# Performance work log

Hardware: AMD Instinct MI355X
Metric: run time of the kernel (lower is better)

## Reference

```python
import jax, jax.numpy as jnp
import numpy as np

FOUR_PI = 4.0 * np.pi
BIG = 1e10


def winding_numbers(points, tris):
    """Generalized winding number of `points` [B,N,3] w.r.t. triangle soup
    `tris` [B,F,3,3], via the Van Oosterom-Strackee solid-angle formula."""
    # vectors from each query point to the three triangle corners: [B,N,F,3]
    a = tris[:, None, :, 0, :] - points[:, :, None, :]
    b = tris[:, None, :, 1, :] - points[:, :, None, :]
    c = tris[:, None, :, 2, :] - points[:, :, None, :]
    la = jnp.linalg.norm(a, axis=-1)
    lb = jnp.linalg.norm(b, axis=-1)
    lc = jnp.linalg.norm(c, axis=-1)
    det = jnp.sum(a * jnp.cross(b, c), axis=-1)  # scalar triple product [B,N,F]
    denom = (la * lb * lc
             + jnp.sum(a * b, axis=-1) * lc
             + jnp.sum(b * c, axis=-1) * la
             + jnp.sum(c * a, axis=-1) * lb)
    omega = 2.0 * jnp.arctan2(det, denom)  # solid angle per triangle
    return jnp.sum(omega, axis=-1) / FOUR_PI  # [B,N]


def pairwise_dist(x, y):
    """Euclidean distances between clouds x [B,N1,3] and y [B,N2,3] -> [B,N1,N2]."""
    sq = (jnp.sum(x * x, -1)[:, :, None]
          + jnp.sum(y * y, -1)[:, None, :]
          - 2.0 * jnp.einsum('bnd,bmd->bnm', x, y))
    return jnp.sqrt(jnp.maximum(sq, 0.0))


def setup_inputs() -> dict:
    key = jax.random.key(0)
    k1, k2, k3 = jax.random.split(key, 3)
    B, N, F = 2, 6890, 3
    NF = 2000
    v1 = jax.random.normal(k1, (B, N, 3), dtype=jnp.float32)
    v2 = jax.random.normal(k2, (B, N, 3), dtype=jnp.float32) + 0.5
    faces = jax.random.randint(k3, (NF, 3), 0, N, dtype=jnp.int32)
    return {"v1": v1, "v2": v2, "faces": faces}


def _masked_stats(row_min, mask):
    # row_min [B,K] minimum distances; mask [B,K] interior flags
    any_in = jnp.any(mask, axis=1)                                   # [B]
    mx = jnp.max(jnp.where(mask, row_min, -BIG), axis=1)
    cnt = jnp.sum(mask, axis=1).astype(row_min.dtype)
    mn = jnp.sum(jnp.where(mask, row_min, 0.0), axis=1) / jnp.maximum(cnt, 1.0)
    zero = jnp.zeros_like(mx)
    return jnp.where(any_in, mx, zero), jnp.where(any_in, mn, zero)


def reference(v1, v2, faces):
    # triangle soups (no mouth-closing: 'smpl' path): [B,F,3,3]
    t1 = v1[:, faces, :]
    t2 = v2[:, faces, :]
    interior_v1 = winding_numbers(v1, t2) >= 0.99  # [B,N1]
    interior_v2 = winding_numbers(v2, t1) >= 0.99  # [B,N2]
    d = pairwise_dist(v1, v2)                      # [B,N1,N2]
    min_dist = jnp.min(d, axis=(1, 2))             # [B]
    row_min = jnp.min(d, axis=2)                   # [B,N1] dist of each v1 to v2
    col_min = jnp.min(d, axis=1)                   # [B,N2] dist of each v2 to v1
    max_12, mean_12 = _masked_stats(row_min, interior_v1)
    max_21, mean_21 = _masked_stats(col_min, interior_v2)
    # stacked [5,B]: min_dist, max_v1_in_v2, mean_v1_in_v2, max_v2_in_v1, mean_v2_in_v1
    return jnp.stack([min_dist, max_12, mean_12, max_21, mean_21], axis=0)
```

## Files before the change

kernel.cpp:

```cpp
#include <hip/hip_runtime.h>
#include <math.h>

#define B_     2
#define N_     6890
#define NF_    2000
#define NFP_   2048
#define NPT_   6912
#define OPP7_  7168
#define TCG_   16
#define OCG_   7
#define NTILE_ (4 * (TCG_ + OCG_) * 27)
#define GRID_  2048

typedef float v2f __attribute__((ext_vector_type(2)));
#define VFMA(a,b,c) __builtin_elementwise_fma((v2f)(a), (v2f)(b), (v2f)(c))

__device__ __forceinline__ float atan2_o2pi(float y, float x) {
    float ax = __builtin_fabsf(x);
    float ay = __builtin_fabsf(y);
    float mx = fmaxf(ax, ay);
    float mn = fminf(ax, ay);
    bool  big = mn > 0.41421356f * mx;
    float num = big ? (mn - mx) : mn;
    float den = big ? (mn + mx) : mx;
    float t   = num * __builtin_amdgcn_rcpf(den);
    float z   = t * t;
    float p   = fmaf(fmaf(fmaf(1.2817932e-2f, z, -2.2087019e-2f), z,
                          3.1795514e-2f), z, -5.3051037e-2f);
    float r   = fmaf(t, fmaf(z, p, 0.15915494309f), big ? 0.125f : 0.0f);
    r = (ay > ax)  ? 0.25f - r : r;
    r = (x < 0.0f) ? 0.5f  - r : r;
    return copysignf(r, y);
}

__global__ void prep_kernel(const float* __restrict__ v1, const float* __restrict__ v2,
                            const int* __restrict__ faces,
                            float4* __restrict__ pw1, float4* __restrict__ pw2,
                            float4* __restrict__ st1, float4* __restrict__ st2,
                            float* __restrict__ tbl1, float* __restrict__ tbl2) {
    int tid = blockIdx.x * 256 + threadIdx.x;

    if (tid < B_ * NPT_) {
        int b = tid / NPT_, n = tid - b * NPT_;
        float4 q1 = make_float4(0.f, 0.f, 0.f, 0.f), q2 = q1;
        if (n < N_) {
            float x1 = v1[(b*N_+n)*3+0], y1 = v1[(b*N_+n)*3+1], z1 = v1[(b*N_+n)*3+2];
            float x2 = v2[(b*N_+n)*3+0], y2 = v2[(b*N_+n)*3+1], z2 = v2[(b*N_+n)*3+2];
            q1 = make_float4(x1, y1, z1, fmaf(x1,x1, fmaf(y1,y1, z1*z1)));
            q2 = make_float4(x2, y2, z2, fmaf(x2,x2, fmaf(y2,y2, z2*z2)));
        }
        pw1[tid] = q1; pw2[tid] = q2;
    }

    if (tid < B_ * OPP7_) {
        int b = tid / OPP7_, n = tid - b * OPP7_;
        float4 q1 = make_float4(0.f, 0.f, 0.f, 1e30f), q2 = q1;
        if (n < N_) {
            float x1 = v1[(b*N_+n)*3+0], y1 = v1[(b*N_+n)*3+1], z1 = v1[(b*N_+n)*3+2];
            float x2 = v2[(b*N_+n)*3+0], y2 = v2[(b*N_+n)*3+1], z2 = v2[(b*N_+n)*3+2];
            q1 = make_float4(-2.f*x1, -2.f*y1, -2.f*z1, fmaf(x1,x1, fmaf(y1,y1, z1*z1)));
            q2 = make_float4(-2.f*x2, -2.f*y2, -2.f*z2, fmaf(x2,x2, fmaf(y2,y2, z2*z2)));
        }
        st1[tid] = q1; st2[tid] = q2;
    }

    if (tid < 2 * B_ * NFP_) {
        int src = tid >> 12;
        int rr  = tid & (B_ * NFP_ - 1);
        int b   = rr >> 11;
        int f   = rr & (NFP_ - 1);
        const float* V = src ? v2 : v1;
        float Ax=1.f,Ay=1.f,Az=1.f,Bx=1.f,By=1.f,Bz=1.f,Cx=1.f,Cy=1.f,Cz=1.f;
        if (f < NF_) {
            int i0 = faces[f*3+0], i1 = faces[f*3+1], i2 = faces[f*3+2];
            Ax=V[(b*N_+i0)*3+0]; Ay=V[(b*N_+i0)*3+1]; Az=V[(b*N_+i0)*3+2];
            Bx=V[(b*N_+i1)*3+0]; By=V[(b*N_+i1)*3+1]; Bz=V[(b*N_+i1)*3+2];
            Cx=V[(b*N_+i2)*3+0]; Cy=V[(b*N_+i2)*3+1]; Cz=V[(b*N_+i2)*3+2];
        }
        float Sx = (Ay*Bz - Az*By) + (By*Cz - Bz*Cy) + (Cy*Az - Cz*Ay);
        float Sy = (Az*Bx - Ax*Bz) + (Bz*Cx - Bx*Cz) + (Cz*Ax - Cx*Az);
        float Sz = (Ax*By - Ay*Bx) + (Bx*Cy - By*Cx) + (Cx*Ay - Cy*Ax);
        float det0 = Ax*(By*Cz - Bz*Cy) + Ay*(Bz*Cx - Bx*Cz) + Az*(Bx*Cy - By*Cx);
        float na = Ax*Ax+Ay*Ay+Az*Az, nb = Bx*Bx+By*By+Bz*Bz, nc = Cx*Cx+Cy*Cy+Cz*Cz;
        float qab = Ax*Bx+Ay*By+Az*Bz, qbc = Bx*Cx+By*Cy+Bz*Cz, qca = Cx*Ax+Cy*Ay+Cz*Az;
        float* o = (src ? tbl2 : tbl1) + ((b << 11) + f) * 20;
        o[0]=Ax;  o[1]=Ay;  o[2]=Az;  o[3]=Bx;  o[4]=By;  o[5]=Bz;
        o[6]=Cx;  o[7]=Cy;  o[8]=Cz;  o[9]=-Sx; o[10]=-Sy; o[11]=-Sz;
        o[12]=det0; o[13]=na; o[14]=nb; o[15]=nc;
        o[16]=qab;  o[17]=qbc; o[18]=qca; o[19]=0.f;
    }
}

__global__ __launch_bounds__(256) void mega_kernel(
        const float4* __restrict__ pw1, const float4* __restrict__ pw2,
        const float* __restrict__ tbl1, const float* __restrict__ tbl2,
        const float4* __restrict__ st1, const float4* __restrict__ st2,
        float* __restrict__ part, float* __restrict__ rmp) {
    __shared__ float4 ptsd[512];
    int t = threadIdx.x, wid = t >> 6, lane = t & 63;
    int pbase = (wid << 7) + lane;
    int srcl = (lane + 1) & 63;

    for (int tile = blockIdx.x; tile < NTILE_; tile += GRID_) {
        int g = tile / 23, o = tile - g * 23;
        __syncthreads();

        if (o < TCG_) {
            int wb   = g * TCG_ + o;
            int pgrp = wb % 27;
            int r    = wb / 27;
            int cg   = r & 15, db = r >> 4;
            int b = db & 1, dir = db >> 1;

            const float4* pw  = dir ? pw2 : pw1;
            const float*  tbl = dir ? tbl1 : tbl2;

            float4 P0 = pw[b * NPT_ + pgrp * 256 + t];
            ptsd[pbase]      = P0;
            ptsd[pbase + 64] = P0;

            const float4* rpA = (const float4*)(tbl + (size_t)(b*NFP_ + cg*128 +   0 + lane)*20);
            const float4* rpB = (const float4*)(tbl + (size_t)(b*NFP_ + cg*128 +  64 + lane)*20);
            float4 a0 = rpA[0], a1 = rpA[1], a2 = rpA[2], a3 = rpA[3], a4 = rpA[4];
            float4 b0 = rpB[0], b1 = rpB[1], b2 = rpB[2], b3 = rpB[3], b4 = rpB[4];
            v2f cAx = {a0.x,b0.x}, cAy = {a0.y,b0.y}, cAz = {a0.z,b0.z};
            v2f cBx = {a0.w,b0.w}, cBy = {a1.x,b1.x}, cBz = {a1.y,b1.y};
            v2f cCx = {a1.z,b1.z}, cCy = {a1.w,b1.w}, cCz = {a2.x,b2.x};
            v2f cSx = {a2.y,b2.y}, cSy = {a2.z,b2.z}, cSz = {a2.w,b2.w};
            v2f cD0 = {a3.x,b3.x}, cNa = {a3.y,b3.y}, cNb = {a3.z,b3.z}, cNc = {a3.w,b3.w};
            v2f cQab= {a4.x,b4.x}, cQbc= {a4.y,b4.y}, cQca= {a4.z,b4.z};
            __syncthreads();

            const float4* mypts = ptsd + pbase;
            float acc = 0.f;
            #pragma unroll 4
            for (int k = 0; k < 64; ++k) {
                float4 P = mypts[k];
                v2f px = P.x, py = P.y, pz = P.z, sv = P.w;
                v2f dAp = VFMA(cAx, px, VFMA(cAy, py, cAz * pz));
                v2f dBp = VFMA(cBx, px, VFMA(cBy, py, cBz * pz));
                v2f dCp = VFMA(cCx, px, VFMA(cCy, py, cCz * pz));
                v2f det = VFMA(cSx, px, VFMA(cSy, py, VFMA(cSz, pz, cD0)));
                v2f la2 = VFMA((v2f)(-2.f), dAp, cNa + sv);
                v2f lb2 = VFMA((v2f)(-2.f), dBp, cNb + sv);
                v2f lc2 = VFMA((v2f)(-2.f), dCp, cNc + sv);
                v2f la, lb, lc;
                la.x = __builtin_amdgcn_sqrtf(fmaxf(la2.x, 0.f));
                la.y = __builtin_amdgcn_sqrtf(fmaxf(la2.y, 0.f));
                lb.x = __builtin_amdgcn_sqrtf(fmaxf(lb2.x, 0.f));
                lb.y = __builtin_amdgcn_sqrtf(fmaxf(lb2.y, 0.f));
                lc.x = __builtin_amdgcn_sqrtf(fmaxf(lc2.x, 0.f));
                lc.y = __builtin_amdgcn_sqrtf(fmaxf(lc2.y, 0.f));
                v2f dab = (cQab + sv) - (dAp + dBp);
                v2f dbc = (cQbc + sv) - (dBp + dCp);
                v2f dca = (cQca + sv) - (dCp + dAp);
                v2f denom = VFMA(VFMA(la, lb, dab), lc, VFMA(dbc, la, dca * lb));
                float g0 = atan2_o2pi(det.x, denom.x);
                float g1 = atan2_o2pi(det.y, denom.y);
                acc += g0 + g1;
                acc = __shfl(acc, srcl, 64);
            }
            part[(db*TCG_ + cg)*NPT_ + pgrp*256 + t] = acc;
        } else {
            int rb   = g * OCG_ + (o - TCG_);
            int pgrp = rb % 27;
            int r    = rb / 27;
            int ocg  = r % OCG_, db = r / OCG_;
            int b = db & 1, dir = db >> 1;

            const float4* pw = dir ? pw2 : pw1;
            const float4* st = dir ? st1 : st2;

            float4 P0 = pw[b * NPT_ + pgrp * 256 + t];
            ptsd[pbase]      = P0;
            ptsd[pbase + 64] = P0;

            const float4* qb = st + b * OPP7_ + ocg * 1024;
#define LQ(j) float4 q##j = qb[j*64 + lane];
            LQ(0) LQ(1) LQ(2) LQ(3) LQ(4) LQ(5) LQ(6) LQ(7)
            LQ(8) LQ(9) LQ(10) LQ(11) LQ(12) LQ(13) LQ(14) LQ(15)
#undef LQ
            __syncthreads();

            const float4* mypts = ptsd + pbase;
            float m = 3.4e38f;
            #pragma unroll 2
            for (int k = 0; k < 64; ++k) {
                float4 P = mypts[k];
                float s = P.w;
#define DD(j) float d##j = fmaf(q##j.x,P.x, fmaf(q##j.y,P.y, fmaf(q##j.z,P.z, q##j.w)));
                DD(0) DD(1) DD(2) DD(3) DD(4) DD(5) DD(6) DD(7)
                DD(8) DD(9) DD(10) DD(11) DD(12) DD(13) DD(14) DD(15)
#undef DD
                float e0 = fminf(d0,d1),  e1 = fminf(d2,d3),  e2 = fminf(d4,d5),  e3 = fminf(d6,d7);
                float e4 = fminf(d8,d9),  e5 = fminf(d10,d11), e6 = fminf(d12,d13), e7 = fminf(d14,d15);
                float f0 = fminf(e0,e1), f1 = fminf(e2,e3), f2 = fminf(e4,e5), f3 = fminf(e6,e7);
                float h  = fminf(fminf(f0,f1), fminf(f2,f3));
                m = fminf(m, h + s);
                m = __shfl(m, srcl, 64);
            }
            rmp[(db*OCG_ + ocg)*NPT_ + pgrp*256 + t] = m;
        }
    }
}

__global__ __launch_bounds__(256) void fold_kernel(
        const float* __restrict__ part, const float* __restrict__ rmp,
        float4* __restrict__ pstat) {
    int pg = blockIdx.x % 27, db = blockIdx.x / 27;
    int t = threadIdx.x, n = pg * 256 + t;

    float ws = 0.f;
    #pragma unroll
    for (int g = 0; g < TCG_; ++g) ws += part[(db*TCG_ + g)*NPT_ + n];
    float rv = 3.4e38f;
    #pragma unroll
    for (int g = 0; g < OCG_; ++g) rv = fminf(rv, rmp[(db*OCG_ + g)*NPT_ + n]);

    bool valid = n < N_;
    float d = sqrtf(rv);
    bool msk = valid && (ws >= 0.99f);
    float v_min = valid ? d : 3.4e38f;
    float v_max = msk ? d : -3.4e38f;
    float v_sum = msk ? d : 0.f;
    float v_cnt = msk ? 1.f : 0.f;

    #pragma unroll
    for (int off = 32; off; off >>= 1) {
        v_min = fminf(v_min, __shfl_down(v_min, off, 64));
        v_max = fmaxf(v_max, __shfl_down(v_max, off, 64));
        v_sum += __shfl_down(v_sum, off, 64);
        v_cnt += __shfl_down(v_cnt, off, 64);
    }
    __shared__ float4 sred[4];
    int wid = t >> 6, lane = t & 63;
    if (lane == 0) sred[wid] = make_float4(v_min, v_max, v_sum, v_cnt);
    __syncthreads();
    if (t == 0) {
        float4 a = sred[0], bb = sred[1], c = sred[2], dd = sred[3];
        pstat[db*27 + pg] = make_float4(
            fminf(fminf(a.x, bb.x), fminf(c.x, dd.x)),
            fmaxf(fmaxf(a.y, bb.y), fmaxf(c.y, dd.y)),
            (a.z + bb.z) + (c.z + dd.z),
            (a.w + bb.w) + (c.w + dd.w));
    }
}

__global__ void final_kernel(const float4* __restrict__ pstat, float* __restrict__ out) {
    int t = threadIdx.x, wid = t >> 6, lane = t & 63;
    float4 v = make_float4(3.4e38f, -3.4e38f, 0.f, 0.f);
    if (lane < 27) v = pstat[wid*27 + lane];
    #pragma unroll
    for (int off = 32; off; off >>= 1) {
        v.x = fminf(v.x, __shfl_down(v.x, off, 64));
        v.y = fmaxf(v.y, __shfl_down(v.y, off, 64));
        v.z += __shfl_down(v.z, off, 64);
        v.w += __shfl_down(v.w, off, 64);
    }
    __shared__ float4 res[4];
    if (lane == 0) res[wid] = v;
    __syncthreads();
    if (t == 0) {
        #pragma unroll
        for (int b = 0; b < B_; ++b) {
            float4 s1 = res[b], s2 = res[2 + b];
            out[0 + b] = s1.x;
            out[2 + b] = (s1.w > 0.f) ? s1.y : 0.f;
            out[4 + b] = (s1.w > 0.f) ? (s1.z / s1.w) : 0.f;
            out[6 + b] = (s2.w > 0.f) ? s2.y : 0.f;
            out[8 + b] = (s2.w > 0.f) ? (s2.z / s2.w) : 0.f;
        }
    }
}

extern "C" void kernel_launch(void* const* d_in, const int* in_sizes, int n_in,
                              void* d_out, int out_size, void* d_ws, size_t ws_size,
                              hipStream_t stream) {
    const float* v1    = (const float*)d_in[0];
    const float* v2    = (const float*)d_in[1];
    const int*   faces = (const int*)d_in[2];

    float4* f4 = (float4*)d_ws;
    float4* pw1   = f4;
    float4* pw2   = pw1 + B_ * NPT_;
    float4* st1   = pw2 + B_ * NPT_;
    float4* st2   = st1 + B_ * OPP7_;
    float4* pstat = st2 + B_ * OPP7_;
    float*  tbl1  = (float*)(pstat + 128);
    float*  tbl2  = tbl1 + B_ * NFP_ * 20;
    float*  part  = tbl2 + B_ * NFP_ * 20;
    float*  rmp   = part + 4 * TCG_ * NPT_;

    float* out = (float*)d_out;

    prep_kernel<<<(B_ * OPP7_ + 255) / 256, 256, 0, stream>>>(
        v1, v2, faces, pw1, pw2, st1, st2, tbl1, tbl2);

    mega_kernel<<<GRID_, 256, 0, stream>>>(
        pw1, pw2, tbl1, tbl2, st1, st2, part, rmp);

    fold_kernel<<<4 * 27, 256, 0, stream>>>(part, rmp, pstat);

    final_kernel<<<1, 256, 0, stream>>>(pstat, out);
}
```

Before: 107.7 us.

## Schedule tiles via atomic work queue and rotate lanes with DPP

Replaces the static grid-stride tile assignment with a global atomic counter. Blocks pull tiles dynamically, and the heavier winding-number tiles are ordered first so the cheaper distance tiles fill in the tail. The per-iteration cross-lane __shfl is replaced by a DPP wave rotate-left, which avoids an LDS permute. The __syncthreads after staging points is also dropped, since each wave only reads its own LDS region. The cost is one extra atomic plus barrier per tile, a counter reset in the prep kernel, and reliance on the DPP rotate matching the old lane direction.

Result: slower. 113.7 us (+5.5%).

```diff
diff --git a/kernel.cpp b/kernel.cpp
--- a/kernel.cpp
+++ b/kernel.cpp
@@ -9,11 +9,17 @@
 #define OPP7_  7168
 #define TCG_   16
 #define OCG_   7
+#define WTILE_ (4 * TCG_ * 27)
 #define NTILE_ (4 * (TCG_ + OCG_) * 27)
 #define GRID_  2048
 
 typedef float v2f __attribute__((ext_vector_type(2)));
 #define VFMA(a,b,c) __builtin_elementwise_fma((v2f)(a), (v2f)(b), (v2f)(c))
+
+__device__ __forceinline__ float rotl1(float v) {
+    return __int_as_float(__builtin_amdgcn_update_dpp(
+        __float_as_int(v), __float_as_int(v), 0x134, 0xF, 0xF, false));
+}
 
 __device__ __forceinline__ float atan2_o2pi(float y, float x) {
     float ax = __builtin_fabsf(x);
@@ -37,8 +43,10 @@
                             const int* __restrict__ faces,
                             float4* __restrict__ pw1, float4* __restrict__ pw2,
                             float4* __restrict__ st1, float4* __restrict__ st2,
-                            float* __restrict__ tbl1, float* __restrict__ tbl2) {
+                            float* __restrict__ tbl1, float* __restrict__ tbl2,
+                            int* __restrict__ cnt) {
     int tid = blockIdx.x * 256 + threadIdx.x;
+    if (tid == 0) *cnt = 0;
 
     if (tid < B_ * NPT_) {
         int b = tid / NPT_, n = tid - b * NPT_;
@@ -95,20 +103,23 @@
         const float4* __restrict__ pw1, const float4* __restrict__ pw2,
         const float* __restrict__ tbl1, const float* __restrict__ tbl2,
         const float4* __restrict__ st1, const float4* __restrict__ st2,
-        float* __restrict__ part, float* __restrict__ rmp) {
+        float* __restrict__ part, float* __restrict__ rmp,
+        int* __restrict__ cnt) {
     __shared__ float4 ptsd[512];
+    __shared__ int stile;
     int t = threadIdx.x, wid = t >> 6, lane = t & 63;
     int pbase = (wid << 7) + lane;
-    int srcl = (lane + 1) & 63;
-
-    for (int tile = blockIdx.x; tile < NTILE_; tile += GRID_) {
-        int g = tile / 23, o = tile - g * 23;
+
+    for (;;) {
         __syncthreads();
-
-        if (o < TCG_) {
-            int wb   = g * TCG_ + o;
-            int pgrp = wb % 27;
-            int r    = wb / 27;
+        if (t == 0) stile = atomicAdd(cnt, 1);
+        __syncthreads();
+        int tile = stile;
+        if (tile >= NTILE_) break;
+
+        if (tile < WTILE_) {
+            int pgrp = tile % 27;
+            int r    = tile / 27;
             int cg   = r & 15, db = r >> 4;
             int b = db & 1, dir = db >> 1;
 
@@ -129,7 +140,6 @@
             v2f cSx = {a2.y,b2.y}, cSy = {a2.z,b2.z}, cSz = {a2.w,b2.w};
             v2f cD0 = {a3.x,b3.x}, cNa = {a3.y,b3.y}, cNb = {a3.z,b3.z}, cNc = {a3.w,b3.w};
             v2f cQab= {a4.x,b4.x}, cQbc= {a4.y,b4.y}, cQca= {a4.z,b4.z};
-            __syncthreads();
 
             const float4* mypts = ptsd + pbase;
             float acc = 0.f;
@@ -157,12 +167,11 @@
                 v2f denom = VFMA(VFMA(la, lb, dab), lc, VFMA(dbc, la, dca * lb));
                 float g0 = atan2_o2pi(det.x, denom.x);
                 float g1 = atan2_o2pi(det.y, denom.y);
-                acc += g0 + g1;
-                acc = __shfl(acc, srcl, 64);
+                acc = rotl1(acc + (g0 + g1));
             }
             part[(db*TCG_ + cg)*NPT_ + pgrp*256 + t] = acc;
         } else {
-            int rb   = g * OCG_ + (o - TCG_);
+            int rb   = tile - WTILE_;
             int pgrp = rb % 27;
             int r    = rb / 27;
             int ocg  = r % OCG_, db = r / OCG_;
@@ -180,7 +189,6 @@
             LQ(0) LQ(1) LQ(2) LQ(3) LQ(4) LQ(5) LQ(6) LQ(7)
             LQ(8) LQ(9) LQ(10) LQ(11) LQ(12) LQ(13) LQ(14) LQ(15)
 #undef LQ
-            __syncthreads();
 
             const float4* mypts = ptsd + pbase;
             float m = 3.4e38f;
@@ -196,8 +204,7 @@
                 float e4 = fminf(d8,d9),  e5 = fminf(d10,d11), e6 = fminf(d12,d13), e7 = fminf(d14,d15);
                 float f0 = fminf(e0,e1), f1 = fminf(e2,e3), f2 = fminf(e4,e5), f3 = fminf(e6,e7);
                 float h  = fminf(fminf(f0,f1), fminf(f2,f3));
-                m = fminf(m, h + s);
-                m = __shfl(m, srcl, 64);
+                m = rotl1(fminf(m, h + s));
             }
             rmp[(db*OCG_ + ocg)*NPT_ + pgrp*256 + t] = m;
         }
@@ -290,14 +297,15 @@
     float*  tbl2  = tbl1 + B_ * NFP_ * 20;
     float*  part  = tbl2 + B_ * NFP_ * 20;
     float*  rmp   = part + 4 * TCG_ * NPT_;
+    int*    cnt   = (int*)(rmp + 4 * OCG_ * NPT_);
 
     float* out = (float*)d_out;
 
     prep_kernel<<<(B_ * OPP7_ + 255) / 256, 256, 0, stream>>>(
-        v1, v2, faces, pw1, pw2, st1, st2, tbl1, tbl2);
+        v1, v2, faces, pw1, pw2, st1, st2, tbl1, tbl2, cnt);
 
     mega_kernel<<<GRID_, 256, 0, stream>>>(
-        pw1, pw2, tbl1, tbl2, st1, st2, part, rmp);
+        pw1, pw2, tbl1, tbl2, st1, st2, part, rmp, cnt);
 
     fold_kernel<<<4 * 27, 256, 0, stream>>>(part, rmp, pstat);
 
```
